# Optimization experiments

Hardware: AMD Instinct MI355X
Metric: run time of the kernel (lower is better)

Reference implementation:

```python
import jax, jax.numpy as jnp
import numpy as np

N_EMBD = 1024
N_HEAD = 16
HEAD_DIM = N_EMBD // N_HEAD


def setup_inputs() -> dict:
    key = jax.random.key(0)
    ks = jax.random.split(key, 9)
    B, T, C = 2, 2048, N_EMBD
    s = 1.0 / np.sqrt(C)
    inp = {
        "x": jax.random.normal(ks[0], (B, T, C), dtype=jnp.float32),
        "Wq": jax.random.normal(ks[1], (C, C), dtype=jnp.float32) * s,
        "bq": jnp.zeros((C,), dtype=jnp.float32),
        "Wk": jax.random.normal(ks[2], (C, C), dtype=jnp.float32) * s,
        "bk": jnp.zeros((C,), dtype=jnp.float32),
        "Wv": jax.random.normal(ks[3], (C, C), dtype=jnp.float32) * s,
        "bv": jnp.zeros((C,), dtype=jnp.float32),
        "Wo": jax.random.normal(ks[4], (C, C), dtype=jnp.float32) * s,
        "bo": jnp.zeros((C,), dtype=jnp.float32),
    }
    return inp


def reference(x, Wq, bq, Wk, bk, Wv, bv, Wo, bo):
    B, T, C = x.shape
    H, D = N_HEAD, HEAD_DIM
    # projections (torch Linear: x @ W^T + b)
    q = (x @ Wq.T + bq).reshape(B, T, H, D).transpose(0, 2, 1, 3)  # [B,H,T,D]
    k = (x @ Wk.T + bk).reshape(B, T, H, D).transpose(0, 2, 1, 3)
    v = (x @ Wv.T + bv).reshape(B, T, H, D).transpose(0, 2, 1, 3)
    scores = jnp.einsum("bhqd,bhkd->bhqk", q, k) / jnp.sqrt(jnp.asarray(D, x.dtype))
    causal = jnp.tril(jnp.ones((T, T), dtype=bool))
    scores = jnp.where(causal[None, None], scores, jnp.asarray(-jnp.inf, x.dtype))
    weights = jax.nn.softmax(scores, axis=-1)  # [B,H,T,T]
    attended = jnp.einsum("bhqk,bhkd->bhqd", weights, v)
    attended = attended.transpose(0, 2, 1, 3).reshape(B, T, C)
    return attended @ Wo.T + bo
```

## Files before the change

### kernel.cpp

```cpp
#include <hip/hip_runtime.h>

typedef unsigned short u16;
typedef __attribute__((ext_vector_type(8))) __bf16 bf16x8;
typedef __attribute__((ext_vector_type(4))) float f32x4;
typedef __attribute__((ext_vector_type(4))) unsigned int u32x4;

#define MFMA16(a, b, c) __builtin_amdgcn_mfma_f32_16x16x32_bf16(a, b, c, 0, 0, 0)

__device__ __forceinline__ u16 f2bf(float f) {
    unsigned u = __float_as_uint(f);
    u = (u + 0x7FFFu + ((u >> 16) & 1u)) >> 16;
    return (u16)u;
}

__device__ __forceinline__ void gl_lds16(const u16* g, u16* l) {
    __builtin_amdgcn_global_load_lds(
        (const __attribute__((address_space(1))) unsigned int*)g,
        (__attribute__((address_space(3))) unsigned int*)l, 16, 0, 0);
}

static constexpr int Bv = 2, Tv = 2048, Cv = 1024, Hv = 16, Dv = 64;
static constexpr int Mv = Bv * Tv;

static constexpr size_t OFF_XB = 0;
static constexpr size_t OFF_WQ = 4194304;
static constexpr size_t OFF_WK = OFF_WQ + 1048576;
static constexpr size_t OFF_WV = OFF_WK + 1048576;
static constexpr size_t OFF_WO = OFF_WV + 1048576;
static constexpr size_t OFF_Q  = OFF_WO + 1048576;
static constexpr size_t OFF_K  = OFF_Q + 4194304;
static constexpr size_t OFF_VT = OFF_K + 4194304;
static constexpr size_t OFF_A  = OFF_VT + 4194304;

__global__ __launch_bounds__(256) void convert_all(
    const float* __restrict__ x,
    const float* __restrict__ wq, const float* __restrict__ wk,
    const float* __restrict__ wv, const float* __restrict__ wo,
    u16* __restrict__ dst)
{
    int i4 = blockIdx.x * blockDim.x + threadIdx.x;
    if (i4 >= 2097152) return;
    int idx = i4 * 4;
    const float* src; int off;
    if (idx < 4194304) { src = x; off = idx; }
    else {
        int rel = idx - 4194304;
        int j = rel >> 20;
        off = rel & 1048575;
        src = (j == 0) ? wq : (j == 1) ? wk : (j == 2) ? wv : wo;
    }
    float4 v = *(const float4*)(src + off);
    ushort4 o;
    o.x = f2bf(v.x); o.y = f2bf(v.y); o.z = f2bf(v.z); o.w = f2bf(v.w);
    *(ushort4*)(dst + idx) = o;
}

template <bool OUT_BF16, bool ROWBIAS>
__device__ __forceinline__ void gemm128_b32(
    u16* __restrict__ lA0, u16* __restrict__ lB0,
    u16* __restrict__ lA1, u16* __restrict__ lB1,
    const u16* __restrict__ A, const u16* __restrict__ Wt,
    const float* __restrict__ bias, void* __restrict__ outp,
    int m0, int n0, int N, int K)
{
    const int tid  = threadIdx.x;
    const int lane = tid & 63, w = tid >> 6;
    const int quad = lane >> 4, lm = lane & 15;
    const int wm = (w & 1) * 64, wn = (w >> 1) * 64;
    const int h4A = (w & 1) * 4, h4B = ((w >> 1) & 1) * 4;
    const int rowi = lane >> 3, seg = lane & 7;
    const int raw = seg ^ rowi;
    const int hh  = raw >> 2, qq = raw & 3;

    f32x4 zero = {0.f, 0.f, 0.f, 0.f};
    f32x4 acc[4][4];
    #pragma unroll
    for (int mt = 0; mt < 4; mt++)
        #pragma unroll
        for (int nt = 0; nt < 4; nt++) acc[mt][nt] = zero;

    auto stage = [&](u16* dA, u16* dB, int k0) __attribute__((always_inline)) {
        #pragma unroll
        for (int j = 0; j < 2; j++) {
            int pr0 = w * 16 + j * 8;
            int gr  = pr0 + rowi + (hh << 6);
            gl_lds16(A  + (size_t)(m0 + gr) * K + k0 + qq * 8, &dA[pr0 * 64]);
            gl_lds16(Wt + (size_t)(n0 + gr) * K + k0 + qq * 8, &dB[pr0 * 64]);
        }
    };
    auto compute = [&](const u16* sA, const u16* sB) __attribute__((always_inline)) {
        bf16x8 af[4], bf[4];
        #pragma unroll
        for (int mt = 0; mt < 4; mt++)
            af[mt] = *(const bf16x8*)&sA[(mt * 16 + lm) * 64 + (((h4A + quad) ^ (lm & 7)) * 8)];
        #pragma unroll
        for (int nt = 0; nt < 4; nt++)
            bf[nt] = *(const bf16x8*)&sB[(nt * 16 + lm) * 64 + (((h4B + quad) ^ (lm & 7)) * 8)];
        #pragma unroll
        for (int mt = 0; mt < 4; mt++)
            #pragma unroll
            for (int nt = 0; nt < 4; nt++)
                acc[mt][nt] = MFMA16(af[mt], bf[nt], acc[mt][nt]);
    };

    const int NT = K >> 5;
    stage(lA0, lB0, 0);
    stage(lA1, lB1, 32);
    for (int t = 0; t < NT; ++t) {
        if (t + 1 < NT) asm volatile("s_waitcnt vmcnt(4)" ::: "memory");
        else            asm volatile("s_waitcnt vmcnt(0)" ::: "memory");
        __builtin_amdgcn_s_barrier();
        const u16* sA = (t & 1) ? lA1 : lA0;
        const u16* sB = (t & 1) ? lB1 : lB0;
        compute(sA, sB);
        asm volatile("s_waitcnt lgkmcnt(0)" ::: "memory");
        __builtin_amdgcn_s_barrier();
        if (t + 2 < NT) stage((t & 1) ? lA1 : lA0, (t & 1) ? lB1 : lB0, (t + 2) << 5);
    }

    #pragma unroll
    for (int nt = 0; nt < 4; nt++) {
        int col = n0 + wn + nt * 16 + lm;
        float cb = ROWBIAS ? 0.f : bias[col];
        #pragma unroll
        for (int mt = 0; mt < 4; mt++) {
            #pragma unroll
            for (int r = 0; r < 4; r++) {
                int row = m0 + wm + mt * 16 + quad * 4 + r;
                float v = acc[mt][nt][r] + (ROWBIAS ? bias[row] : cb);
                if (OUT_BF16) ((u16*)outp)[(size_t)row * N + col] = f2bf(v);
                else          ((float*)outp)[(size_t)row * N + col] = v;
            }
        }
    }
}

__global__ __launch_bounds__(256, 3) void gemm_qkv(
    const u16* __restrict__ A,
    const u16* __restrict__ Wq, const u16* __restrict__ Wk, const u16* __restrict__ Wv,
    const float* __restrict__ bq, const float* __restrict__ bk, const float* __restrict__ bv,
    u16* __restrict__ Q, u16* __restrict__ K, u16* __restrict__ VT)
{
    __shared__ u16 lA0[64 * 64];
    __shared__ u16 lB0[64 * 64];
    __shared__ u16 lA1[64 * 64];
    __shared__ u16 lB1[64 * 64];

    int bid = blockIdx.x;
    int sw  = (bid & 7) * 96 + (bid >> 3);
    int g2  = sw >> 5;
    int row = sw & 31;
    int which = g2 >> 3, col = g2 & 7;

    if (which == 0) {
        gemm128_b32<true, false>(lA0, lB0, lA1, lB1, A, Wq, bq, Q, row * 128, col * 128, Cv, Cv);
    } else if (which == 1) {
        gemm128_b32<true, false>(lA0, lB0, lA1, lB1, A, Wk, bk, K, row * 128, col * 128, Cv, Cv);
    } else {
        gemm128_b32<true, true>(lA0, lB0, lA1, lB1, Wv, A, bv, VT, col * 128, row * 128, Mv, Cv);
    }
}

__global__ __launch_bounds__(256, 3) void gemm_o64(
    const u16* __restrict__ A, const u16* __restrict__ Wt,
    const float* __restrict__ bias, float* __restrict__ outp)
{
    __shared__ u16 lA0[64 * 64];
    __shared__ u16 lB0[64 * 64];
    __shared__ u16 lA1[64 * 64];
    __shared__ u16 lB1[64 * 64];

    int bid = blockIdx.x;
    int sw  = (bid & 7) * 32 + (bid >> 3);
    int col = sw >> 5;
    int row = sw & 31;

    gemm128_b32<false, false>(lA0, lB0, lA1, lB1, A, Wt, bias, outp,
                              row * 128, col * 128, Cv, Cv);
}

__global__ __launch_bounds__(512) void attn(
    const u16* __restrict__ Qp, const u16* __restrict__ Kp,
    const u16* __restrict__ VTg, u16* __restrict__ Op)
{
    __shared__ u16 lK[2][64 * 64];
    __shared__ u16 lVT[2][64 * 64];
    __shared__ u16 lP[8][32][72];

    const int tid  = threadIdx.x;
    const int lane = tid & 63, w = tid >> 6;
    const int g = w >> 2, wl = w & 3;
    const int quad = lane >> 4, lm = lane & 15;

    const int idx  = blockIdx.x;
    const int half = idx >> 8;
    const int grp  = idx & 255;
    const int bh   = (half << 4) | (grp >> 4);
    const int j    = grp & 15;
    const int qt   = half ? j : 15 - j;
    const int h = bh & 15, b = bh >> 4;

    const int qb = qt * 128;
    const size_t headoff = (size_t)b * Tv * Cv + (size_t)h * Dv;
    const size_t vthead  = (size_t)h * 64 * Mv + (size_t)b * Tv;

    bf16x8 qf[2][2];
    #pragma unroll
    for (int nt = 0; nt < 2; nt++) {
        const u16* qptr = Qp + headoff + (size_t)(qb + wl * 32 + nt * 16 + lm) * Cv + quad * 8;
        qf[0][nt] = *(const bf16x8*)(qptr);
        qf[1][nt] = *(const bf16x8*)(qptr + 32);
    }

    f32x4 zero = {0.f, 0.f, 0.f, 0.f};
    f32x4 oacc[2][4];
    #pragma unroll
    for (int mt = 0; mt < 2; mt++)
        #pragma unroll
        for (int nt = 0; nt < 4; nt++) oacc[mt][nt] = zero;
    float Lp[2] = {0.f, 0.f};

    const float SC = 0.18033688011112042f;
    const int rowi = lane >> 3, seg = lane & 7;

    auto stage = [&](int kt) {
        const int k0 = kt * 64;
        #pragma unroll
        for (int hf = 0; hf < 2; hf++) {
            int rbase = wl * 16 + hf * 8;
            int row = rbase + rowi;
            int gseg = seg ^ (row & 7);
            gl_lds16(Kp + headoff + (size_t)(k0 + row) * Cv + gseg * 8, &lK[g][rbase * 64]);
            gl_lds16(VTg + vthead + (size_t)row * Mv + k0 + gseg * 8, &lVT[g][rbase * 64]);
        }
    };

    auto body = [&](int kt, bool domask) __attribute__((always_inline)) {
        const int k0 = kt * 64;
        f32x4 stt[4][2];
        #pragma unroll
        for (int mt = 0; mt < 4; mt++)
            #pragma unroll
            for (int nt = 0; nt < 2; nt++) stt[mt][nt] = zero;
        __builtin_amdgcn_s_setprio(1);
        #pragma unroll
        for (int ks = 0; ks < 2; ks++) {
            #pragma unroll
            for (int mt = 0; mt < 4; mt++) {
                bf16x8 kf = *(const bf16x8*)
                    &lK[g][(mt * 16 + lm) * 64 + (((ks * 4 + quad) ^ (lm & 7)) * 8)];
                #pragma unroll
                for (int nt = 0; nt < 2; nt++)
                    stt[mt][nt] = MFMA16(kf, qf[ks][nt], stt[mt][nt]);
            }
        }
        __builtin_amdgcn_s_setprio(0);
        #pragma unroll
        for (int mt = 0; mt < 4; mt++) {
            #pragma unroll
            for (int nt = 0; nt < 2; nt++) {
                const int keyb = k0 + mt * 16 + quad * 4;
                const int qrow = qb + wl * 32 + nt * 16 + lm;
                float e0 = __builtin_amdgcn_exp2f(fmaf(stt[mt][nt][0], SC, -16.f));
                float e1 = __builtin_amdgcn_exp2f(fmaf(stt[mt][nt][1], SC, -16.f));
                float e2 = __builtin_amdgcn_exp2f(fmaf(stt[mt][nt][2], SC, -16.f));
                float e3 = __builtin_amdgcn_exp2f(fmaf(stt[mt][nt][3], SC, -16.f));
                if (domask) {
                    if (keyb + 0 > qrow) e0 = 0.f;
                    if (keyb + 1 > qrow) e1 = 0.f;
                    if (keyb + 2 > qrow) e2 = 0.f;
                    if (keyb + 3 > qrow) e3 = 0.f;
                }
                Lp[nt] += e0 + e1 + e2 + e3;
                ushort4 pk;
                pk.x = (u16)(__float_as_uint(e0) >> 16);
                pk.y = (u16)(__float_as_uint(e1) >> 16);
                pk.z = (u16)(__float_as_uint(e2) >> 16);
                pk.w = (u16)(__float_as_uint(e3) >> 16);
                *(ushort4*)&lP[w][nt * 16 + lm][mt * 16 + quad * 4] = pk;
            }
        }
        __builtin_amdgcn_s_setprio(1);
        #pragma unroll
        for (int ks = 0; ks < 2; ks++) {
            bf16x8 pf[2];
            #pragma unroll
            for (int mt = 0; mt < 2; mt++)
                pf[mt] = *(const bf16x8*)&lP[w][mt * 16 + lm][ks * 32 + quad * 8];
            #pragma unroll
            for (int nt = 0; nt < 4; nt++) {
                bf16x8 vf = *(const bf16x8*)
                    &lVT[g][(nt * 16 + lm) * 64 + (((ks * 4 + quad) ^ (lm & 7)) * 8)];
                #pragma unroll
                for (int mt = 0; mt < 2; mt++)
                    oacc[mt][nt] = MFMA16(pf[mt], vf, oacc[mt][nt]);
            }
        }
        __builtin_amdgcn_s_setprio(0);
    };

    for (int i = 0; i < qt; i++) {
        if (i) __syncthreads();
        stage(2 * i + g);
        __syncthreads();
        body(2 * i + g, false);
    }
    if (qt) __syncthreads();
    stage(2 * qt + g);
    __syncthreads();
    body(2 * qt + g, true);
    __syncthreads();

    float* lO = (float*)&lP[0][0][0];
    float* lL = lO + 32 * 256;
    const int t = tid & 255;
    if (g == 1) {
        #pragma unroll
        for (int mt = 0; mt < 2; mt++)
            #pragma unroll
            for (int nt = 0; nt < 4; nt++)
                #pragma unroll
                for (int r = 0; r < 4; r++)
                    lO[(mt * 16 + nt * 4 + r) * 256 + t] = oacc[mt][nt][r];
        lL[t] = Lp[0];
        lL[256 + t] = Lp[1];
    }
    __syncthreads();
    if (g == 0) {
        #pragma unroll
        for (int mt = 0; mt < 2; mt++)
            #pragma unroll
            for (int nt = 0; nt < 4; nt++)
                #pragma unroll
                for (int r = 0; r < 4; r++)
                    oacc[mt][nt][r] += lO[(mt * 16 + nt * 4 + r) * 256 + t];
        Lp[0] += lL[t];
        Lp[1] += lL[256 + t];

        float Lred[2];
        #pragma unroll
        for (int nt = 0; nt < 2; nt++) {
            float L = Lp[nt];
            L += __shfl_xor(L, 16, 64);
            L += __shfl_xor(L, 32, 64);
            Lred[nt] = 1.0f / L;
        }
        #pragma unroll
        for (int mt = 0; mt < 2; mt++) {
            float inv[4];
            #pragma unroll
            for (int r = 0; r < 4; r++)
                inv[r] = __shfl(Lred[mt], (lane & 48) | (quad * 4 + r), 64);
            #pragma unroll
            for (int nt = 0; nt < 4; nt++) {
                #pragma unroll
                for (int r = 0; r < 4; r++) {
                    int row = qb + wl * 32 + mt * 16 + quad * 4 + r;
                    Op[headoff + (size_t)row * Cv + nt * 16 + lm] = f2bf(oacc[mt][nt][r] * inv[r]);
                }
            }
        }
    }
}

extern "C" void kernel_launch(void* const* d_in, const int* in_sizes, int n_in,
                              void* d_out, int out_size, void* d_ws, size_t ws_size,
                              hipStream_t stream) {
    const float* x  = (const float*)d_in[0];
    const float* Wq = (const float*)d_in[1];
    const float* bq = (const float*)d_in[2];
    const float* Wk = (const float*)d_in[3];
    const float* bk = (const float*)d_in[4];
    const float* Wv = (const float*)d_in[5];
    const float* bv = (const float*)d_in[6];
    const float* Wo = (const float*)d_in[7];
    const float* bo = (const float*)d_in[8];
    u16* ws = (u16*)d_ws;

    convert_all<<<8192, 256, 0, stream>>>(x, Wq, Wk, Wv, Wo, ws);

    gemm_qkv<<<768, 256, 0, stream>>>(
        ws + OFF_XB, ws + OFF_WQ, ws + OFF_WK, ws + OFF_WV,
        bq, bk, bv, ws + OFF_Q, ws + OFF_K, ws + OFF_VT);

    attn<<<512, 512, 0, stream>>>(ws + OFF_Q, ws + OFF_K, ws + OFF_VT, ws + OFF_A);

    gemm_o64<<<256, 256, 0, stream>>>(ws + OFF_A, ws + OFF_WO, bo, (float*)d_out);
}
```

Before: 175.7 us.

## Rewrite QKV projection GEMM with 256x256 tiles and 512-thread blocks

Replaces the 128x128-tile QKV GEMM (768 blocks of 256 threads) with a dedicated 256x256-tile kernel that uses 8 waves per block, BK=64 and double-buffered LDS staging via global_load_lds. Larger tiles are meant to raise arithmetic intensity and cut redundant global loads of A and W. In exchange, only 192 blocks are launched on a 256-CU device, so some CUs sit idle. The 128 KB of LDS and the 128 accumulator registers per thread also limit occupancy.

```diff
diff --git a/kernel.cpp b/kernel.cpp
--- a/kernel.cpp
+++ b/kernel.cpp
@@ -55,6 +55,105 @@
     *(ushort4*)(dst + idx) = o;
 }
 
+__global__ __launch_bounds__(512) void gemm_qkv(
+    const u16* __restrict__ A,
+    const u16* __restrict__ Wq, const u16* __restrict__ Wk, const u16* __restrict__ Wv,
+    const float* __restrict__ bq, const float* __restrict__ bk, const float* __restrict__ bv,
+    u16* __restrict__ Q, u16* __restrict__ K, u16* __restrict__ VT)
+{
+    __shared__ u16 lA[2][256 * 64];
+    __shared__ u16 lB[2][256 * 64];
+
+    const int bid = blockIdx.x;
+    const int which = bid >> 6, sub = bid & 63;
+    const u16* Ap; const u16* Wt; const float* bias; u16* out;
+    int m0, n0, outN; bool rowbias;
+    if (which == 0) {
+        Ap = A; Wt = Wq; bias = bq; out = Q;
+        m0 = (sub >> 2) * 256; n0 = (sub & 3) * 256; outN = Cv; rowbias = false;
+    } else if (which == 1) {
+        Ap = A; Wt = Wk; bias = bk; out = K;
+        m0 = (sub >> 2) * 256; n0 = (sub & 3) * 256; outN = Cv; rowbias = false;
+    } else {
+        Ap = Wv; Wt = A; bias = bv; out = VT;
+        m0 = (sub & 3) * 256; n0 = (sub >> 2) * 256; outN = Mv; rowbias = true;
+    }
+    const int Kd = Cv;
+
+    const int tid  = threadIdx.x;
+    const int lane = tid & 63, w = tid >> 6;
+    const int wr = w >> 2, wc = w & 3;
+    const int quad = lane >> 4, lm = lane & 15;
+    const int rowi = lane >> 3, seg = lane & 7;
+    const int gsg8 = (seg ^ rowi) * 8;
+
+    f32x4 zero = {0.f, 0.f, 0.f, 0.f};
+    f32x4 acc[8][4];
+    #pragma unroll
+    for (int mf = 0; mf < 8; mf++)
+        #pragma unroll
+        for (int nf = 0; nf < 4; nf++) acc[mf][nf] = zero;
+
+    auto stageT = [&](int b, int k0) __attribute__((always_inline)) {
+        #pragma unroll
+        for (int j = 0; j < 4; j++) {
+            int r8 = (w + j * 8) * 8;
+            gl_lds16(Ap + (size_t)(m0 + r8 + rowi) * Kd + k0 + gsg8, &lA[b][r8 * 64]);
+            gl_lds16(Wt + (size_t)(n0 + r8 + rowi) * Kd + k0 + gsg8, &lB[b][r8 * 64]);
+        }
+    };
+    auto computeT = [&](int b) __attribute__((always_inline)) {
+        #pragma unroll
+        for (int ks = 0; ks < 2; ks++) {
+            const int swz = ((ks * 4 + quad) ^ (lm & 7)) * 8;
+            bf16x8 bf[4];
+            #pragma unroll
+            for (int nf = 0; nf < 4; nf++)
+                bf[nf] = *(const bf16x8*)&lB[b][(wc * 64 + nf * 16 + lm) * 64 + swz];
+            #pragma unroll
+            for (int mq = 0; mq < 2; mq++) {
+                bf16x8 af[4];
+                #pragma unroll
+                for (int i = 0; i < 4; i++)
+                    af[i] = *(const bf16x8*)&lA[b][(wr * 128 + mq * 64 + i * 16 + lm) * 64 + swz];
+                #pragma unroll
+                for (int i = 0; i < 4; i++)
+                    #pragma unroll
+                    for (int nf = 0; nf < 4; nf++)
+                        acc[mq * 4 + i][nf] = MFMA16(af[i], bf[nf], acc[mq * 4 + i][nf]);
+            }
+        }
+    };
+
+    const int NT = Kd >> 6;
+    stageT(0, 0);
+    stageT(1, 64);
+    for (int t = 0; t < NT; ++t) {
+        if (t + 1 < NT) asm volatile("s_waitcnt vmcnt(8)" ::: "memory");
+        else            asm volatile("s_waitcnt vmcnt(0)" ::: "memory");
+        __builtin_amdgcn_s_barrier();
+        computeT(t & 1);
+        asm volatile("s_waitcnt lgkmcnt(0)" ::: "memory");
+        __builtin_amdgcn_s_barrier();
+        if (t + 2 < NT) stageT(t & 1, (t + 2) << 6);
+    }
+
+    #pragma unroll
+    for (int nf = 0; nf < 4; nf++) {
+        int col = n0 + wc * 64 + nf * 16 + lm;
+        float cb = rowbias ? 0.f : bias[col];
+        #pragma unroll
+        for (int mf = 0; mf < 8; mf++) {
+            #pragma unroll
+            for (int r = 0; r < 4; r++) {
+                int row = m0 + wr * 128 + mf * 16 + quad * 4 + r;
+                float v = acc[mf][nf][r] + (rowbias ? bias[row] : cb);
+                out[(size_t)row * outN + col] = f2bf(v);
+            }
+        }
+    }
+}
+
 template <bool OUT_BF16, bool ROWBIAS>
 __device__ __forceinline__ void gemm128_b32(
     u16* __restrict__ lA0, u16* __restrict__ lB0,
@@ -132,32 +231,6 @@
                 else          ((float*)outp)[(size_t)row * N + col] = v;
             }
         }
-    }
-}
-
-__global__ __launch_bounds__(256, 3) void gemm_qkv(
-    const u16* __restrict__ A,
-    const u16* __restrict__ Wq, const u16* __restrict__ Wk, const u16* __restrict__ Wv,
-    const float* __restrict__ bq, const float* __restrict__ bk, const float* __restrict__ bv,
-    u16* __restrict__ Q, u16* __restrict__ K, u16* __restrict__ VT)
-{
-    __shared__ u16 lA0[64 * 64];
-    __shared__ u16 lB0[64 * 64];
-    __shared__ u16 lA1[64 * 64];
-    __shared__ u16 lB1[64 * 64];
-
-    int bid = blockIdx.x;
-    int sw  = (bid & 7) * 96 + (bid >> 3);
-    int g2  = sw >> 5;
-    int row = sw & 31;
-    int which = g2 >> 3, col = g2 & 7;
-
-    if (which == 0) {
-        gemm128_b32<true, false>(lA0, lB0, lA1, lB1, A, Wq, bq, Q, row * 128, col * 128, Cv, Cv);
-    } else if (which == 1) {
-        gemm128_b32<true, false>(lA0, lB0, lA1, lB1, A, Wk, bk, K, row * 128, col * 128, Cv, Cv);
-    } else {
-        gemm128_b32<true, true>(lA0, lB0, lA1, lB1, Wv, A, bv, VT, col * 128, row * 128, Mv, Cv);
     }
 }
 
@@ -379,7 +452,7 @@
 
     convert_all<<<8192, 256, 0, stream>>>(x, Wq, Wk, Wv, Wo, ws);
 
-    gemm_qkv<<<768, 256, 0, stream>>>(
+    gemm_qkv<<<192, 512, 0, stream>>>(
         ws + OFF_XB, ws + OFF_WQ, ws + OFF_WK, ws + OFF_WV,
         bq, bk, bv, ws + OFF_Q, ws + OFF_K, ws + OFF_VT);
 
```

Result: slower. 191.0 us (+8.7%).
